# Kernel tuning notes

Measured on AMD Instinct MI355X. Metric: run time of the kernel, lower is better.

The kernel has to match this reference:

```python
import jax, jax.numpy as jnp
import numpy as np

NUM_HEADS = 16


def setup_inputs() -> dict:
    key = jax.random.key(0)
    ks = jax.random.split(key, 8)
    B, S, E = 2, 2048, 1024
    w_scale = 0.02  # xavier-ish init scale
    return {
        "x": jax.random.normal(ks[0], (B, S, E), dtype=jnp.float32),
        "qkv_w": jax.random.normal(ks[1], (3 * E, E), dtype=jnp.float32) * w_scale,
        "qkv_b": jnp.zeros((3 * E,), dtype=jnp.float32),
        "out_w": jax.random.normal(ks[2], (E, E), dtype=jnp.float32) * w_scale,
        "out_b": jnp.zeros((E,), dtype=jnp.float32),
        "head_gates": jax.random.normal(ks[3], (NUM_HEADS,), dtype=jnp.float32) + 1.0,
        "head_importance": jax.random.normal(ks[4], (NUM_HEADS,), dtype=jnp.float32) + 1.0,
        "head_threshold": jax.random.uniform(ks[5], (), dtype=jnp.float32),
    }


def reference(x, qkv_w, qkv_b, out_w, out_b, head_gates, head_importance, head_threshold):
    B, S, E = x.shape
    H = NUM_HEADS
    D = E // H
    # dynamic head selection: gate score vs learned threshold -> binary per-head mask
    gate_score = jax.nn.sigmoid(head_gates * head_importance)          # [H]
    active_heads = (gate_score > head_threshold).astype(x.dtype)       # [H]

    qkv = x @ qkv_w.T + qkv_b                                          # [B,S,3E]
    qkv = qkv.reshape(B, S, 3, H, D).transpose(2, 0, 3, 1, 4)          # [3,B,H,S,D]
    qkv = qkv * active_heads[None, None, :, None, None]                # mask inactive heads
    q, k, v = qkv[0], qkv[1], qkv[2]

    # NOTE: source computes scale = sqrt(head_dim) but never applies it -> unscaled scores
    scores = jnp.einsum('bhsd,bhtd->bhst', q, k)                       # [B,H,S,S]
    attn = jax.nn.softmax(scores, axis=-1)
    out = jnp.einsum('bhst,bhtd->bhsd', attn, v)
    out = out + v.mean(axis=2, keepdims=True)                          # residual mean of v over seq

    out = out.transpose(0, 2, 1, 3).reshape(B, S, E)
    return out @ out_w.T + out_b
```

## Files before the change

### kernel.cpp

```cpp
#include <hip/hip_runtime.h>

#define BB 2
#define SS 2048
#define EE 1024
#define HH 16
#define DD_ 64
#define BH (BB*HH)
#define NQKV (3*EE)
#define MROWS (BB*SS)

typedef _Float16 f16;
typedef _Float16 f16x8 __attribute__((ext_vector_type(8)));
typedef _Float16 f16x4 __attribute__((ext_vector_type(4)));
typedef __fp16 fp16x2 __attribute__((ext_vector_type(2)));
typedef float f32x4 __attribute__((ext_vector_type(4)));
typedef float f32x16 __attribute__((ext_vector_type(16)));

#define MFMA16(a,b,c) __builtin_amdgcn_mfma_f32_16x16x32_f16(a,b,c,0,0,0)
#define MFMA32(a,b,c) __builtin_amdgcn_mfma_f32_32x32x16_f16(a,b,c,0,0,0)
#define EXP2F(x) __builtin_amdgcn_exp2f(x)
#define LOG2E 1.44269504088896f

__device__ __forceinline__ bool head_active(
    const float* gates, const float* imp, const float* thr, int h) {
    const float gs = 1.f / (1.f + __expf(-gates[h] * imp[h]));
    return gs > thr[0];
}

__device__ __forceinline__ void gload16(const void* g, void* l) {
    __builtin_amdgcn_global_load_lds(
        (const __attribute__((address_space(1))) void*)g,
        (__attribute__((address_space(3))) void*)l, 16, 0, 0);
}

__device__ __forceinline__ float vmax16(f32x16 v) {
    float a = fmaxf(v[0], v[1]),  b = fmaxf(v[2], v[3]);
    float c = fmaxf(v[4], v[5]),  d = fmaxf(v[6], v[7]);
    float e = fmaxf(v[8], v[9]),  f = fmaxf(v[10], v[11]);
    float g = fmaxf(v[12], v[13]), h = fmaxf(v[14], v[15]);
    a = fmaxf(a, b); c = fmaxf(c, d); e = fmaxf(e, f); g = fmaxf(g, h);
    return fmaxf(fmaxf(a, c), fmaxf(e, g));
}

#define NX4  1048576
#define NW14  786432
#define NW24  262144
__global__ __launch_bounds__(256) void cvt_kernel(
    const float* __restrict__ x, const float* __restrict__ w1,
    const float* __restrict__ w2, f16* __restrict__ x16,
    f16* __restrict__ w116, f16* __restrict__ w216,
    const float* __restrict__ gates, const float* __restrict__ imp,
    const float* __restrict__ thr)
{
    const int i = blockIdx.x * 256 + threadIdx.x;
    const float* src; f16* dst; int off;
    if (i < NX4)              { src = x;  dst = x16;  off = i; }
    else if (i < NX4 + NW14)  {
        src = w1; dst = w116; off = i - NX4;
        const int row = off >> 8;
        if (!head_active(gates, imp, thr, (row & 1023) >> 6)) return;
    }
    else                      { src = w2; dst = w216; off = i - NX4 - NW14; }
    float4 v = ((const float4*)src)[off];
    f16x4 h = { (f16)v.x, (f16)v.y, (f16)v.z, (f16)v.w };
    *(f16x4*)(dst + 4*(size_t)off) = h;
}

__global__ __launch_bounds__(256) void qkv_gemm_kernel(
    const f16* __restrict__ x, const f16* __restrict__ w,
    const float* __restrict__ bias, const float* __restrict__ gates,
    const float* __restrict__ imp, const float* __restrict__ thr,
    f16* __restrict__ q16, f16* __restrict__ k16, f16* __restrict__ v16)
{
    __shared__ f16 As[128*64];
    __shared__ f16 Bs[64*64];
    const int tid  = threadIdx.x;
    const int wave = tid >> 6, lane = tid & 63;
    const int quad = lane >> 4, l15 = lane & 15;
    const int m0 = blockIdx.x << 7;
    const int n0 = blockIdx.y << 6;
    const int which = n0 >> 10;
    const int h     = (n0 & 1023) >> 6;
    if (!head_active(gates, imp, thr, h)) return;

    f32x4 acc[2][4];
#pragma unroll
    for (int i = 0; i < 2; ++i)
#pragma unroll
        for (int j = 0; j < 4; ++j) acc[i][j] = (f32x4){0.f,0.f,0.f,0.f};

    for (int k0 = 0; k0 < EE; k0 += 64) {
        __syncthreads();
#pragma unroll
        for (int u = 0; u < 4; ++u) {
            const int s = tid + (u << 8);
            const int r = s >> 3;
            const int sc = ((s & 7) ^ (r & 7)) << 3;
            gload16(x + (size_t)(m0 + r)*EE + k0 + sc, &As[s << 3]);
        }
#pragma unroll
        for (int u = 0; u < 2; ++u) {
            const int s = tid + (u << 8);
            const int r = s >> 3;
            const int sc = ((s & 7) ^ (r & 7)) << 3;
            gload16(w + (size_t)(n0 + r)*EE + k0 + sc, &Bs[s << 3]);
        }
        __syncthreads();
#pragma unroll
        for (int ks = 0; ks < 2; ++ks) {
            f16x8 af[2], bf[4];
#pragma unroll
            for (int i = 0; i < 2; ++i) {
                const int r = wave*32 + i*16 + l15;
                af[i] = *(const f16x8*)&As[(r << 6) + ((((ks<<2)+quad) ^ (l15 & 7)) << 3)];
            }
#pragma unroll
            for (int j = 0; j < 4; ++j) {
                const int r = j*16 + l15;
                bf[j] = *(const f16x8*)&Bs[(r << 6) + ((((ks<<2)+quad) ^ (l15 & 7)) << 3)];
            }
#pragma unroll
            for (int i = 0; i < 2; ++i)
#pragma unroll
                for (int j = 0; j < 4; ++j)
                    acc[i][j] = MFMA16(af[i], bf[j], acc[i][j]);
        }
    }

    const float scale = (which == 0) ? LOG2E : 1.f;
    f16* __restrict__ dst = (which == 0) ? q16 : ((which == 1) ? k16 : v16);
    float bv[4];
#pragma unroll
    for (int j = 0; j < 4; ++j) bv[j] = bias[n0 + j*16 + l15];
#pragma unroll
    for (int i = 0; i < 2; ++i) {
#pragma unroll
        for (int reg = 0; reg < 4; ++reg) {
            const int m = m0 + wave*32 + i*16 + quad*4 + reg;
            const int b = m >> 11, s = m & (SS - 1);
            f16* rowp = dst + (((size_t)(b*HH + h))*SS + s)*DD_ + l15;
#pragma unroll
            for (int j = 0; j < 4; ++j)
                rowp[j*16] = (f16)((acc[i][j][reg] + bv[j]) * scale);
        }
    }
}

__global__ __launch_bounds__(256) void vtrans_kernel(
    const f16* __restrict__ v16, f16* __restrict__ vt, float* __restrict__ vmean,
    const float* __restrict__ gates, const float* __restrict__ imp,
    const float* __restrict__ thr)
{
    const int bh = blockIdx.y;
    if (!head_active(gates, imp, thr, bh & (HH - 1))) return;
    __shared__ f16 T[64][74];
    const int tid = threadIdx.x;
    const int s0 = blockIdx.x << 6;
#pragma unroll
    for (int u = 0; u < 2; ++u) {
        const int f = tid + (u << 8);
        const int r = f >> 3, c = (f & 7) << 3;
        *(f16x8*)&T[r][c] = *(const f16x8*)(v16 + ((size_t)bh*SS + s0 + r)*DD_ + c);
    }
    __syncthreads();
    const int d = tid >> 2, ch = (tid & 3) << 4;
    union { f16 h[16]; f16x8 v8[2]; } t;
    float ps = 0.f;
#pragma unroll
    for (int u = 0; u < 16; ++u) { f16 val = T[ch + u][d]; t.h[u] = val; ps += (float)val; }
    f16* dp = vt + ((size_t)bh*DD_ + d)*SS + s0 + ch;
    *(f16x8*)(dp)     = t.v8[0];
    *(f16x8*)(dp + 8) = t.v8[1];
    ps += __shfl_xor(ps, 1, 64);
    ps += __shfl_xor(ps, 2, 64);
    if ((tid & 3) == 0) atomicAdd(vmean + bh*DD_ + d, ps * (1.f / SS));
}

template<int KPL>
__global__ __launch_bounds__(256, 4) void attn_kernel(
    const f16* __restrict__ q16, const f16* __restrict__ k16,
    const f16* __restrict__ vt,
    const float* __restrict__ gates, const float* __restrict__ imp,
    const float* __restrict__ thr,
    float* __restrict__ opart, float* __restrict__ mlpart)
{
    constexpr int NT = 1 << (5 - KPL);
    __shared__ f16 Ks[2][64*64];
    __shared__ f16 Vs[2][64*64];
    const int tid  = threadIdx.x;
    const int wave = tid >> 6, lane = tid & 63;
    const int l31 = lane & 31, hi = lane >> 5, l7 = lane & 7;
    const int bh = blockIdx.y;
    const int kp = blockIdx.x & ((1 << KPL) - 1);
    const int qc = blockIdx.x >> KPL;
    const int q0 = qc << 7;
    const int k0 = kp << (11 - KPL);

    if (!head_active(gates, imp, thr, bh & (HH - 1))) return;

    const f16* qb = q16 + (size_t)bh * SS * DD_;
    const f16* kb = k16 + (size_t)bh * SS * DD_;
    const f16* vb = vt  + (size_t)bh * DD_ * SS;

    const int r0 = tid >> 3, r1 = r0 + 32, cc = tid & 7;
    const int sc0 = (cc ^ (r0 & 7)) << 3;
    const int sc1 = (cc ^ (r1 & 7)) << 3;

    gload16(kb + (size_t)(k0 + r0)*DD_ + sc0, &Ks[0][tid << 3]);
    gload16(kb + (size_t)(k0 + r1)*DD_ + sc1, &Ks[0][(tid + 256) << 3]);
    gload16(vb + (size_t)r0*SS + k0 + sc0,    &Vs[0][tid << 3]);
    gload16(vb + (size_t)r1*SS + k0 + sc1,    &Vs[0][(tid + 256) << 3]);

    f16x8 qf[4];
#pragma unroll
    for (int ks = 0; ks < 4; ++ks)
        qf[ks] = *(const f16x8*)(qb +
            (size_t)(q0 + wave*32 + l31)*DD_ + ks*16 + hi*8);

    f32x16 accO[2];
#pragma unroll
    for (int dt = 0; dt < 2; ++dt)
#pragma unroll
        for (int r = 0; r < 16; ++r) accO[dt][r] = 0.f;
    float M = 0.f;
    float lsum = 0.f;

    int cur = 0;
    for (int t = 0; t < NT; ++t) {
        const int kt = k0 + (t << 6);
        __syncthreads();
        if (t < NT - 1) {
            const int kn = kt + 64;
            gload16(kb + (size_t)(kn + r0)*DD_ + sc0, &Ks[cur^1][tid << 3]);
            gload16(kb + (size_t)(kn + r1)*DD_ + sc1, &Ks[cur^1][(tid + 256) << 3]);
            gload16(vb + (size_t)r0*SS + kn + sc0,    &Vs[cur^1][tid << 3]);
            gload16(vb + (size_t)r1*SS + kn + sc1,    &Vs[cur^1][(tid + 256) << 3]);
        }

        f32x16 accS[2];
        const float negM = -M;
#pragma unroll
        for (int mt = 0; mt < 2; ++mt)
#pragma unroll
            for (int r = 0; r < 16; ++r) accS[mt][r] = negM;
        __builtin_amdgcn_s_setprio(1);
#pragma unroll
        for (int ks = 0; ks < 4; ++ks)
#pragma unroll
            for (int mt = 0; mt < 2; ++mt) {
                f16x8 kf = *(const f16x8*)&Ks[cur][((mt*32 + l31) << 6) +
                                                  ((((ks<<1)+hi) ^ l7) << 3)];
                accS[mt] = MFMA32(kf, qf[ks], accS[mt]);
            }
        __builtin_amdgcn_s_setprio(0);

        const float mxl = fmaxf(vmax16(accS[0]), vmax16(accS[1]));
        if (!__all(mxl <= 8.f)) {
            float mx = mxl;
            mx = fmaxf(mx, __shfl_xor(mx, 1, 64));
            mx = fmaxf(mx, __shfl_xor(mx, 2, 64));
            mx = fmaxf(mx, __shfl_xor(mx, 4, 64));
            mx = fmaxf(mx, __shfl_xor(mx, 8, 64));
            mx = fmaxf(mx, __shfl_xor(mx, 16, 64));
            mx = fmaxf(mx, __shfl_xor(mx, 32, 64));
            const float alpha = EXP2F(-mx);
            M += mx;
            lsum *= alpha;
#pragma unroll
            for (int r = 0; r < 16; ++r) { accO[0][r] *= alpha; accO[1][r] *= alpha; }
#pragma unroll
            for (int mt = 0; mt < 2; ++mt)
#pragma unroll
                for (int r = 0; r < 16; ++r) accS[mt][r] -= mx;
        }

        float rs[2];
#pragma unroll
        for (int mt = 0; mt < 2; ++mt) {
            float t0 = 0.f, t1 = 0.f, t2 = 0.f, t3 = 0.f;
#pragma unroll
            for (int r = 0; r < 16; r += 4) {
                float p0 = EXP2F(accS[mt][r+0]); accS[mt][r+0] = p0; t0 += p0;
                float p1 = EXP2F(accS[mt][r+1]); accS[mt][r+1] = p1; t1 += p1;
                float p2 = EXP2F(accS[mt][r+2]); accS[mt][r+2] = p2; t2 += p2;
                float p3 = EXP2F(accS[mt][r+3]); accS[mt][r+3] = p3; t3 += p3;
            }
            rs[mt] = (t0 + t1) + (t2 + t3);
        }
        float sum = rs[0] + rs[1];
        sum += __shfl_xor(sum, 32, 64);
        lsum += sum;

        int pki[2][8];
#pragma unroll
        for (int mt = 0; mt < 2; ++mt)
#pragma unroll
            for (int t2_ = 0; t2_ < 8; ++t2_) {
                union { fp16x2 h; int i; } c;
                c.h = __builtin_amdgcn_cvt_pkrtz(accS[mt][2*t2_], accS[mt][2*t2_+1]);
                pki[mt][t2_] = c.i;
            }

#pragma unroll
        for (int ks = 0; ks < 4; ++ks) {
            const int mt = ks >> 1;
            const int bidx = (ks & 1) << 2;
            const int a0 = pki[mt][bidx+0], a1 = pki[mt][bidx+1];
            const int b0 = pki[mt][bidx+2], b1 = pki[mt][bidx+3];
            const int s0 = hi ? a0 : b0;
            const int s1 = hi ? a1 : b1;
            const int r0x = __shfl_xor(s0, 32, 64);
            const int r1x = __shfl_xor(s1, 32, 64);
            union { int i[4]; f16x8 h; } u;
            u.i[0] = hi ? r0x : a0;
            u.i[1] = hi ? r1x : a1;
            u.i[2] = hi ? b0 : r0x;
            u.i[3] = hi ? b1 : r1x;
            f16x8 pf = u.h;
            __builtin_amdgcn_s_setprio(1);
#pragma unroll
            for (int dt = 0; dt < 2; ++dt) {
                f16x8 vf = *(const f16x8*)&Vs[cur][((dt*32 + l31) << 6) +
                                                  ((((ks<<1)+hi) ^ l7) << 3)];
                accO[dt] = MFMA32(vf, pf, accO[dt]);
            }
            __builtin_amdgcn_s_setprio(0);
        }
        cur ^= 1;
    }

    {
        const int s = q0 + wave*32 + l31;
        const size_t rowi = (size_t)kp*BH*SS + (size_t)bh*SS + s;
        float* ob = opart + (rowi << 6);
#pragma unroll
        for (int dt = 0; dt < 2; ++dt)
#pragma unroll
            for (int g = 0; g < 4; ++g) {
                const int d0 = dt*32 + 8*g + 4*hi;
                float4 o = { accO[dt][4*g+0], accO[dt][4*g+1],
                             accO[dt][4*g+2], accO[dt][4*g+3] };
                *(float4*)(ob + d0) = o;
            }
        if (hi == 0) {
            float2 ml = { M, lsum };
            *(float2*)(mlpart + rowi*2) = ml;
        }
    }
}

template<int PARTS>
__global__ __launch_bounds__(256) void combine_kernel(
    const float* __restrict__ opart, const float* __restrict__ mlpart,
    const float* __restrict__ vmean,
    const float* __restrict__ gates, const float* __restrict__ imp,
    const float* __restrict__ thr, f16* __restrict__ aout)
{
    const int t = blockIdx.x * 256 + threadIdx.x;
    const int row = t >> 2;
    const int dc = (t & 3) << 4;
    const int bh = row >> 11, s = row & (SS - 1);
    const int b = bh >> 4, h = bh & (HH - 1);
    f16* op = aout + ((size_t)(b*SS + s))*EE + h*DD_ + dc;

    if (!head_active(gates, imp, thr, h)) {
        const f16x4 z = {(f16)0.f, (f16)0.f, (f16)0.f, (f16)0.f};
#pragma unroll
        for (int j = 0; j < 4; ++j) *(f16x4*)(op + 4*j) = z;
        return;
    }

    float2 ml[PARTS];
    float mx = -1.0e30f;
#pragma unroll
    for (int p = 0; p < PARTS; ++p) {
        ml[p] = ((const float2*)mlpart)[(size_t)p*BH*SS + row];
        mx = fmaxf(mx, ml[p].x);
    }
    float a[PARTS], denom = 0.f;
#pragma unroll
    for (int p = 0; p < PARTS; ++p) {
        a[p] = EXP2F(ml[p].x - mx);
        denom += ml[p].y * a[p];
    }
    const float inv = 1.f / denom;
    const float* o0 = opart + ((size_t)row << 6) + dc;
#pragma unroll
    for (int j = 0; j < 4; ++j) {
        float4 acc = {0.f, 0.f, 0.f, 0.f};
#pragma unroll
        for (int p = 0; p < PARTS; ++p) {
            float4 v = ((const float4*)(o0 + (size_t)p*BH*SS*DD_))[j];
            acc.x += v.x*a[p]; acc.y += v.y*a[p];
            acc.z += v.z*a[p]; acc.w += v.w*a[p];
        }
        float4 vm = *(const float4*)(vmean + bh*DD_ + dc + 4*j);
        f16x4 o = { (f16)(acc.x*inv + vm.x), (f16)(acc.y*inv + vm.y),
                    (f16)(acc.z*inv + vm.z), (f16)(acc.w*inv + vm.w) };
        *(f16x4*)(op + 4*j) = o;
    }
}

__global__ __launch_bounds__(256) void out_gemm_kernel(
    const f16* __restrict__ a, const f16* __restrict__ w,
    const float* __restrict__ bias, const float* __restrict__ gates,
    const float* __restrict__ imp, const float* __restrict__ thr,
    float* __restrict__ y)
{
    __shared__ f16 As[128*64];
    __shared__ f16 Bs[128*64];
    const int tid  = threadIdx.x;
    const int wave = tid >> 6, lane = tid & 63;
    const int quad = lane >> 4, l15 = lane & 15;
    const int wm = wave & 1, wn = wave >> 1;
    const int m0 = blockIdx.y << 7, n0 = blockIdx.x << 7;

    unsigned hmask = 0;
#pragma unroll
    for (int h = 0; h < HH; ++h)
        if (head_active(gates, imp, thr, h)) hmask |= (1u << h);

    f32x4 acc[4][4];
#pragma unroll
    for (int i = 0; i < 4; ++i)
#pragma unroll
        for (int j = 0; j < 4; ++j) acc[i][j] = (f32x4){0.f,0.f,0.f,0.f};

    for (int k0 = 0; k0 < EE; k0 += 64) {
        if (!((hmask >> (k0 >> 6)) & 1u)) continue;
        __syncthreads();
#pragma unroll
        for (int u = 0; u < 4; ++u) {
            const int s = tid + (u << 8);
            const int r = s >> 3;
            const int sc = ((s & 7) ^ (r & 7)) << 3;
            gload16(a + (size_t)(m0 + r)*EE + k0 + sc, &As[s << 3]);
            gload16(w + (size_t)(n0 + r)*EE + k0 + sc, &Bs[s << 3]);
        }
        __syncthreads();
#pragma unroll
        for (int ks = 0; ks < 2; ++ks) {
            f16x8 af[4], bf[4];
#pragma unroll
            for (int i = 0; i < 4; ++i) {
                const int r = wm*64 + i*16 + l15;
                af[i] = *(const f16x8*)&As[(r << 6) + ((((ks<<2)+quad) ^ (l15 & 7)) << 3)];
            }
#pragma unroll
            for (int j = 0; j < 4; ++j) {
                const int r = wn*64 + j*16 + l15;
                bf[j] = *(const f16x8*)&Bs[(r << 6) + ((((ks<<2)+quad) ^ (l15 & 7)) << 3)];
            }
#pragma unroll
            for (int i = 0; i < 4; ++i)
#pragma unroll
                for (int j = 0; j < 4; ++j)
                    acc[i][j] = MFMA16(af[i], bf[j], acc[i][j]);
        }
    }

    float bv[4];
#pragma unroll
    for (int j = 0; j < 4; ++j) bv[j] = bias[n0 + wn*64 + j*16 + l15];
#pragma unroll
    for (int i = 0; i < 4; ++i) {
#pragma unroll
        for (int reg = 0; reg < 4; ++reg) {
            const int m = m0 + wm*64 + i*16 + quad*4 + reg;
#pragma unroll
            for (int j = 0; j < 4; ++j)
                y[(size_t)m*EE + n0 + wn*64 + j*16 + l15] = acc[i][j][reg] + bv[j];
        }
    }
}

extern "C" void kernel_launch(void* const* d_in, const int* in_sizes, int n_in,
                              void* d_out, int out_size, void* d_ws, size_t ws_size,
                              hipStream_t stream)
{
    const float* x      = (const float*)d_in[0];
    const float* qkv_w  = (const float*)d_in[1];
    const float* qkv_b  = (const float*)d_in[2];
    const float* out_w  = (const float*)d_in[3];
    const float* out_b  = (const float*)d_in[4];
    const float* gates  = (const float*)d_in[5];
    const float* imp    = (const float*)d_in[6];
    const float* thr    = (const float*)d_in[7];
    float* out = (float*)d_out;

    const size_t TSZ = (size_t)BH * SS * DD_;
    f16* x16  = (f16*)d_ws;
    f16* w116 = x16 + (size_t)MROWS * EE;
    f16* w216 = w116 + (size_t)NQKV * EE;
    f16* q16  = w216 + (size_t)EE * EE;
    f16* k16  = q16 + TSZ;
    f16* v16  = k16 + TSZ;
    f16* vtb  = v16 + TSZ;
    f16* aout = vtb + TSZ;
    float* vmean  = (float*)(aout + TSZ);
    float* opart  = vmean + (size_t)BH * DD_;

    const size_t base_bytes = (size_t)((char*)opart - (char*)d_ws);
    const size_t per_part   = (size_t)BH*SS*DD_*4 + (size_t)BH*SS*2*4;
    const int parts = (ws_size >= base_bytes + 4*per_part) ? 4 : 2;

    float* mlpart = opart + (size_t)parts*BH*SS*DD_;

    (void)hipMemsetAsync(vmean, 0, (size_t)BH * DD_ * sizeof(float), stream);

    cvt_kernel<<<(NX4 + NW14 + NW24) / 256, 256, 0, stream>>>(
        x, qkv_w, out_w, x16, w116, w216, gates, imp, thr);

    dim3 g1(MROWS/128, NQKV/64);
    qkv_gemm_kernel<<<g1, 256, 0, stream>>>(x16, w116, qkv_b, gates, imp, thr,
                                            q16, k16, v16);
    dim3 g2(SS/64, BH);
    vtrans_kernel<<<g2, 256, 0, stream>>>(v16, vtb, vmean, gates, imp, thr);

    dim3 g2a(16 * parts, BH);
    if (parts == 4)
        attn_kernel<2><<<g2a, 256, 0, stream>>>(q16, k16, vtb, gates, imp, thr,
                                                opart, mlpart);
    else
        attn_kernel<1><<<g2a, 256, 0, stream>>>(q16, k16, vtb, gates, imp, thr,
                                                opart, mlpart);

    if (parts == 4)
        combine_kernel<4><<<(BH*SS*4)/256, 256, 0, stream>>>(
            opart, mlpart, vmean, gates, imp, thr, aout);
    else
        combine_kernel<2><<<(BH*SS*4)/256, 256, 0, stream>>>(
            opart, mlpart, vmean, gates, imp, thr, aout);

    dim3 g3(EE/128, MROWS/128);
    out_gemm_kernel<<<g3, 256, 0, stream>>>(aout, w216, out_b, gates, imp, thr,
                                            out);
}
```

Baseline: 167.4 us.

## Double-buffer LDS tiles in QKV and output GEMMs to overlap loads with MFMA

Both GEMM kernels now use two shared-memory buffers and issue the next K-tile's global-to-LDS loads before computing on the current tile. This drops one barrier per iteration and overlaps memory latency with MFMA work. The output GEMM walks only active heads through a bitmask iterator. The combine kernel no longer writes zeros for inactive heads, which is safe because the output GEMM skips those K ranges. This doubles LDS usage and may lower occupancy. Correctness depends on gload16 being synchronous or on the single barrier being enough to order overwrites of the other buffer.

New measurement: 162.6 us. 2.9% less time.

```diff
diff --git a/kernel.cpp b/kernel.cpp
--- a/kernel.cpp
+++ b/kernel.cpp
@@ -72,8 +72,8 @@
     const float* __restrict__ imp, const float* __restrict__ thr,
     f16* __restrict__ q16, f16* __restrict__ k16, f16* __restrict__ v16)
 {
-    __shared__ f16 As[128*64];
-    __shared__ f16 Bs[64*64];
+    __shared__ f16 As[2][128*64];
+    __shared__ f16 Bs[2][64*64];
     const int tid  = threadIdx.x;
     const int wave = tid >> 6, lane = tid & 63;
     const int quad = lane >> 4, l15 = lane & 15;
@@ -83,41 +83,45 @@
     const int h     = (n0 & 1023) >> 6;
     if (!head_active(gates, imp, thr, h)) return;
 
+#define QSTAGE(K0, B) do {                                                   \
+    _Pragma("unroll")                                                        \
+    for (int u = 0; u < 4; ++u) {                                            \
+        const int s_ = tid + (u << 8);                                       \
+        const int r_ = s_ >> 3;                                              \
+        const int sc_ = ((s_ & 7) ^ (r_ & 7)) << 3;                          \
+        gload16(x + (size_t)(m0 + r_)*EE + (K0) + sc_, &As[B][s_ << 3]);     \
+    }                                                                        \
+    _Pragma("unroll")                                                        \
+    for (int u = 0; u < 2; ++u) {                                            \
+        const int s_ = tid + (u << 8);                                       \
+        const int r_ = s_ >> 3;                                              \
+        const int sc_ = ((s_ & 7) ^ (r_ & 7)) << 3;                          \
+        gload16(w + (size_t)(n0 + r_)*EE + (K0) + sc_, &Bs[B][s_ << 3]);     \
+    } } while (0)
+
     f32x4 acc[2][4];
 #pragma unroll
     for (int i = 0; i < 2; ++i)
 #pragma unroll
         for (int j = 0; j < 4; ++j) acc[i][j] = (f32x4){0.f,0.f,0.f,0.f};
 
-    for (int k0 = 0; k0 < EE; k0 += 64) {
+    QSTAGE(0, 0);
+    int cur = 0;
+    for (int t = 0; t < 16; ++t) {
         __syncthreads();
-#pragma unroll
-        for (int u = 0; u < 4; ++u) {
-            const int s = tid + (u << 8);
-            const int r = s >> 3;
-            const int sc = ((s & 7) ^ (r & 7)) << 3;
-            gload16(x + (size_t)(m0 + r)*EE + k0 + sc, &As[s << 3]);
-        }
-#pragma unroll
-        for (int u = 0; u < 2; ++u) {
-            const int s = tid + (u << 8);
-            const int r = s >> 3;
-            const int sc = ((s & 7) ^ (r & 7)) << 3;
-            gload16(w + (size_t)(n0 + r)*EE + k0 + sc, &Bs[s << 3]);
-        }
-        __syncthreads();
+        if (t < 15) QSTAGE((t + 1) << 6, cur ^ 1);
 #pragma unroll
         for (int ks = 0; ks < 2; ++ks) {
             f16x8 af[2], bf[4];
 #pragma unroll
             for (int i = 0; i < 2; ++i) {
                 const int r = wave*32 + i*16 + l15;
-                af[i] = *(const f16x8*)&As[(r << 6) + ((((ks<<2)+quad) ^ (l15 & 7)) << 3)];
+                af[i] = *(const f16x8*)&As[cur][(r << 6) + ((((ks<<2)+quad) ^ (l15 & 7)) << 3)];
             }
 #pragma unroll
             for (int j = 0; j < 4; ++j) {
                 const int r = j*16 + l15;
-                bf[j] = *(const f16x8*)&Bs[(r << 6) + ((((ks<<2)+quad) ^ (l15 & 7)) << 3)];
+                bf[j] = *(const f16x8*)&Bs[cur][(r << 6) + ((((ks<<2)+quad) ^ (l15 & 7)) << 3)];
             }
 #pragma unroll
             for (int i = 0; i < 2; ++i)
@@ -125,7 +129,9 @@
                 for (int j = 0; j < 4; ++j)
                     acc[i][j] = MFMA16(af[i], bf[j], acc[i][j]);
         }
-    }
+        cur ^= 1;
+    }
+#undef QSTAGE
 
     const float scale = (which == 0) ? LOG2E : 1.f;
     f16* __restrict__ dst = (which == 0) ? q16 : ((which == 1) ? k16 : v16);
@@ -361,15 +367,10 @@
     const int dc = (t & 3) << 4;
     const int bh = row >> 11, s = row & (SS - 1);
     const int b = bh >> 4, h = bh & (HH - 1);
+
+    if (!head_active(gates, imp, thr, h)) return;
+
     f16* op = aout + ((size_t)(b*SS + s))*EE + h*DD_ + dc;
-
-    if (!head_active(gates, imp, thr, h)) {
-        const f16x4 z = {(f16)0.f, (f16)0.f, (f16)0.f, (f16)0.f};
-#pragma unroll
-        for (int j = 0; j < 4; ++j) *(f16x4*)(op + 4*j) = z;
-        return;
-    }
-
     float2 ml[PARTS];
     float mx = -1.0e30f;
 #pragma unroll
@@ -407,8 +408,8 @@
     const float* __restrict__ imp, const float* __restrict__ thr,
     float* __restrict__ y)
 {
-    __shared__ f16 As[128*64];
-    __shared__ f16 Bs[128*64];
+    __shared__ f16 As[2][128*64];
+    __shared__ f16 Bs[2][128*64];
     const int tid  = threadIdx.x;
     const int wave = tid >> 6, lane = tid & 63;
     const int quad = lane >> 4, l15 = lane & 15;
@@ -420,36 +421,44 @@
     for (int h = 0; h < HH; ++h)
         if (head_active(gates, imp, thr, h)) hmask |= (1u << h);
 
+#define OSTAGE(K0, B) do {                                                   \
+    _Pragma("unroll")                                                        \
+    for (int u = 0; u < 4; ++u) {                                            \
+        const int s_ = tid + (u << 8);                                       \
+        const int r_ = s_ >> 3;                                              \
+        const int sc_ = ((s_ & 7) ^ (r_ & 7)) << 3;                          \
+        gload16(a + (size_t)(m0 + r_)*EE + (K0) + sc_, &As[B][s_ << 3]);     \
+        gload16(w + (size_t)(n0 + r_)*EE + (K0) + sc_, &Bs[B][s_ << 3]);     \
+    } } while (0)
+
     f32x4 acc[4][4];
 #pragma unroll
     for (int i = 0; i < 4; ++i)
 #pragma unroll
         for (int j = 0; j < 4; ++j) acc[i][j] = (f32x4){0.f,0.f,0.f,0.f};
 
-    for (int k0 = 0; k0 < EE; k0 += 64) {
-        if (!((hmask >> (k0 >> 6)) & 1u)) continue;
+    unsigned m = hmask;
+    int kcur = m ? (__ffs(m) - 1) : -1;
+    if (m) m &= m - 1;
+    if (kcur >= 0) OSTAGE(kcur << 6, 0);
+    int cur = 0;
+    while (kcur >= 0) {
+        const int knext = m ? (__ffs(m) - 1) : -1;
+        if (m) m &= m - 1;
         __syncthreads();
-#pragma unroll
-        for (int u = 0; u < 4; ++u) {
-            const int s = tid + (u << 8);
-            const int r = s >> 3;
-            const int sc = ((s & 7) ^ (r & 7)) << 3;
-            gload16(a + (size_t)(m0 + r)*EE + k0 + sc, &As[s << 3]);
-            gload16(w + (size_t)(n0 + r)*EE + k0 + sc, &Bs[s << 3]);
-        }
-        __syncthreads();
+        if (knext >= 0) OSTAGE(knext << 6, cur ^ 1);
 #pragma unroll
         for (int ks = 0; ks < 2; ++ks) {
             f16x8 af[4], bf[4];
 #pragma unroll
             for (int i = 0; i < 4; ++i) {
                 const int r = wm*64 + i*16 + l15;
-                af[i] = *(const f16x8*)&As[(r << 6) + ((((ks<<2)+quad) ^ (l15 & 7)) << 3)];
+                af[i] = *(const f16x8*)&As[cur][(r << 6) + ((((ks<<2)+quad) ^ (l15 & 7)) << 3)];
             }
 #pragma unroll
             for (int j = 0; j < 4; ++j) {
                 const int r = wn*64 + j*16 + l15;
-                bf[j] = *(const f16x8*)&Bs[(r << 6) + ((((ks<<2)+quad) ^ (l15 & 7)) << 3)];
+                bf[j] = *(const f16x8*)&Bs[cur][(r << 6) + ((((ks<<2)+quad) ^ (l15 & 7)) << 3)];
             }
 #pragma unroll
             for (int i = 0; i < 4; ++i)
@@ -457,7 +466,10 @@
                 for (int j = 0; j < 4; ++j)
                     acc[i][j] = MFMA16(af[i], bf[j], acc[i][j]);
         }
-    }
+        cur ^= 1;
+        kcur = knext;
+    }
+#undef OSTAGE
 
     float bv[4];
 #pragma unroll
@@ -466,10 +478,10 @@
     for (int i = 0; i < 4; ++i) {
 #pragma unroll
         for (int reg = 0; reg < 4; ++reg) {
-            const int m = m0 + wm*64 + i*16 + quad*4 + reg;
+            const int m2 = m0 + wm*64 + i*16 + quad*4 + reg;
 #pragma unroll
             for (int j = 0; j < 4; ++j)
-                y[(size_t)m*EE + n0 + wn*64 + j*16 + l15] = acc[i][j][reg] + bv[j];
+                y[(size_t)m2*EE + n0 + wn*64 + j*16 + l15] = acc[i][j][reg] + bv[j];
         }
     }
 }
```
